# Kernel optimization log

Measured on AMD Instinct MI355X. Metric: run time of the kernel, lower is better.

Reference implementation:

```python
import jax, jax.numpy as jnp
import numpy as np

STRIDES = (8, 16, 32, 64)
NUM_HEADS = 8
G = 4
P = 32
TAU_Z = 2.0
LVL_BASE = 3.0  # stride 8 == 2**3 maps to level 0


def decode_box(xyzr):
    scale = jnp.exp2(xyzr[..., 2:3])
    ratio = jnp.exp2(jnp.concatenate([-0.5 * xyzr[..., 3:4], 0.5 * xyzr[..., 3:4]], axis=-1))
    wh = scale * ratio
    xy = xyzr[..., 0:2]
    return jnp.concatenate([xy - 0.5 * wh, xy + 0.5 * wh], axis=-1)


def position_embedding(box, num_feats, temperature=10000.0):
    term = jnp.array([1000.0, 1000.0, 1.0, 1.0], dtype=box.dtype)
    token = box / term
    dim_t = jnp.arange(num_feats, dtype=jnp.float32)
    dim_t = temperature ** (2.0 * (dim_t // 2) / num_feats)
    pos = token[..., None] / dim_t  # B,N,4,F
    pos = jnp.stack([jnp.sin(pos[..., 0::2]), jnp.cos(pos[..., 1::2])], axis=4)
    B, N = box.shape[:2]
    return pos.reshape(B, N, -1)  # B,N,4*F


def bbox_iof(boxes):
    # boxes: B,N,4 x1y1x2y2; iof[b,i,j] = inter(i,j) / area(i)
    area = jnp.clip(boxes[..., 2] - boxes[..., 0], 0.0) * jnp.clip(boxes[..., 3] - boxes[..., 1], 0.0)
    lt = jnp.maximum(boxes[:, :, None, :2], boxes[:, None, :, :2])
    rb = jnp.minimum(boxes[:, :, None, 2:], boxes[:, None, :, 2:])
    wh = jnp.clip(rb - lt, 0.0)
    inter = wh[..., 0] * wh[..., 1]
    return inter / jnp.clip(area[:, :, None], 1e-7, None)


def bilinear_group_sample(feat, xy, stride):
    # feat: [B,C,H,W]; xy: [B,N,P,G,2] image coords -> [B,N,G,P,C//G]
    B, C, H, W = feat.shape
    _, N, Pn, Gn, _ = xy.shape
    Cg = C // Gn
    featg = feat.reshape(B, Gn, Cg, H * W).transpose(0, 1, 3, 2)  # B,G,HW,Cg
    px = xy[..., 0] / stride - 0.5  # grid_sample align_corners=False convention
    py = xy[..., 1] / stride - 0.5
    x0 = jnp.floor(px)
    y0 = jnp.floor(py)
    bi = jnp.arange(B)[:, None, None]
    gi = jnp.arange(Gn)[None, :, None]
    out = jnp.zeros((B, Gn, N * Pn, Cg), dtype=feat.dtype)
    for dx in (0.0, 1.0):
        for dy in (0.0, 1.0):
            xi = x0 + dx
            yi = y0 + dy
            wgt = (1.0 - jnp.abs(px - xi)) * (1.0 - jnp.abs(py - yi))
            valid = (xi >= 0) & (xi <= W - 1) & (yi >= 0) & (yi <= H - 1)
            wgt = wgt * valid  # zero padding outside
            xi_c = jnp.clip(xi, 0, W - 1).astype(jnp.int32)
            yi_c = jnp.clip(yi, 0, H - 1).astype(jnp.int32)
            idx = (yi_c * W + xi_c).transpose(0, 3, 1, 2).reshape(B, Gn, N * Pn)
            vals = featg[bi, gi, idx]  # B,G,N*P,Cg
            w = wgt.transpose(0, 3, 1, 2).reshape(B, Gn, N * Pn, 1)
            out = out + vals * w
    return out.reshape(B, Gn, N, Pn, Cg).transpose(0, 2, 1, 3, 4)


def layer_norm(x, g, b, eps=1e-5):
    mu = jnp.mean(x, axis=-1, keepdims=True)
    var = jnp.mean((x - mu) ** 2, axis=-1, keepdims=True)
    return (x - mu) * jax.lax.rsqrt(var + eps) * g + b


def _forward(feats, query_content, query_box, Wq, bq, Wk, bk, Wv, bv, Wo, bo,
             ln_g, ln_b, off_W, off_b, sc_W, sc_b, iof_tau):
    B, N, C = query_content.shape
    H = NUM_HEADS
    dh = C // H
    box_cxcy = query_box[..., :2]
    zc = query_box[..., 2:3]
    rc = query_box[..., 3:4]
    box_wh = jnp.exp2(zc) * jnp.exp2(jnp.concatenate([-0.5 * rc, 0.5 * rc], axis=-1))
    logscale = zc.reshape(B, N, 1, 1)

    # torch.no_grad() block -> stop_gradient
    rois = decode_box(query_box)
    iof = jnp.log(bbox_iof(jax.lax.stop_gradient(rois)) + 1e-7)  # B,N,N
    pe = jax.lax.stop_gradient(position_embedding(query_box, C // 4))  # B,N,C
    attn_bias = iof[:, None, :, :] * iof_tau.reshape(1, -1, 1, 1)  # B,H,N,N

    x = query_content + pe
    q = (x @ Wq.T + bq).reshape(B, N, H, dh)
    k = (x @ Wk.T + bk).reshape(B, N, H, dh)
    v = (x @ Wv.T + bv).reshape(B, N, H, dh)
    scores = jnp.einsum('bnhd,bmhd->bhnm', q, k) * (dh ** -0.5) + attn_bias
    attn = jax.nn.softmax(scores, axis=-1)
    ctx = jnp.einsum('bhnm,bmhd->bnhd', attn, v).reshape(B, N, C)
    qc = x + ctx @ Wo.T + bo  # mmcv MultiheadAttention adds identity (= query+pe)
    qc = layer_norm(qc, ln_g, ln_b)

    offset = (qc @ off_W.T + off_b).reshape(B, N, P, G, 2)
    scale_logit = (qc @ sc_W.T + sc_b).reshape(B, N, P, G)
    sample_xy = box_cxcy.reshape(B, N, 1, 1, 2) + offset * box_wh.reshape(B, N, 1, 1, 2)
    sample_z = scale_logit + logscale  # B,N,P,G
    lvl = sample_z - LVL_BASE
    levels = jnp.arange(len(STRIDES), dtype=jnp.float32)
    zw = jax.nn.softmax(-((lvl[..., None] - levels) ** 2) / TAU_Z, axis=-1)  # B,N,P,G,L
    zw_t = zw.transpose(0, 1, 3, 2, 4)  # B,N,G,P,L
    sample_feats = jnp.zeros(())
    for l, (fm, s) in enumerate(zip(feats, STRIDES)):
        sample_feats = sample_feats + bilinear_group_sample(fm, sample_xy, s) * zw_t[..., l:l + 1]
    return sample_feats, sample_xy, offset, sample_z, scale_logit, qc


def setup_inputs():
    key = jax.random.key(0)
    ks = jax.random.split(key, 20)
    B, N, C = 4, 500, 256
    feat0 = jax.random.normal(ks[0], (B, C, 128, 128), dtype=jnp.float32)
    feat1 = jax.random.normal(ks[1], (B, C, 64, 64), dtype=jnp.float32)
    feat2 = jax.random.normal(ks[2], (B, C, 32, 32), dtype=jnp.float32)
    feat3 = jax.random.normal(ks[3], (B, C, 16, 16), dtype=jnp.float32)
    query_content = jax.random.normal(ks[4], (B, N, C), dtype=jnp.float32)
    xy = jax.random.uniform(ks[5], (B, N, 2), minval=64.0, maxval=960.0)
    zz = jax.random.uniform(ks[6], (B, N, 1), minval=3.0, maxval=6.0)
    rr = jax.random.uniform(ks[7], (B, N, 1), minval=-1.0, maxval=1.0)
    query_box = jnp.concatenate([xy, zz, rr], axis=-1)
    sub_query_xy = jax.random.normal(ks[8], (B, N, P, G, 2), dtype=jnp.float32) * 0.1
    sub_query_z = jax.random.normal(ks[9], (B, N, P, G, 4), dtype=jnp.float32) * 0.1
    sub_query_vec = jax.random.normal(ks[10], (B, N, P, G, 64), dtype=jnp.float32) * 0.1
    imgs_whwh = jnp.full((B, N, 4), 1024.0, dtype=jnp.float32)
    w = lambda i, sh: jax.random.normal(ks[i], sh, dtype=jnp.float32) * 0.02
    return {
        'feat0': feat0, 'feat1': feat1, 'feat2': feat2, 'feat3': feat3,
        'query_content': query_content, 'query_box': query_box,
        'sub_query_xy': sub_query_xy, 'sub_query_z': sub_query_z,
        'sub_query_vec': sub_query_vec, 'imgs_whwh': imgs_whwh,
        'Wq': w(11, (C, C)), 'bq': jnp.zeros((C,), jnp.float32),
        'Wk': w(12, (C, C)), 'bk': jnp.zeros((C,), jnp.float32),
        'Wv': w(13, (C, C)), 'bv': jnp.zeros((C,), jnp.float32),
        'Wo': w(14, (C, C)), 'bo': jnp.zeros((C,), jnp.float32),
        'ln_g': jnp.ones((C,), jnp.float32), 'ln_b': jnp.zeros((C,), jnp.float32),
        'off_W': w(15, (2 * G * P, C)),
        'off_b': jax.random.uniform(ks[16], (2 * G * P,), minval=-0.5, maxval=0.5),
        'sc_W': w(17, (G * P, C)),
        'sc_b': jax.random.normal(ks[18], (G * P,), dtype=jnp.float32) * 0.1,
        'iof_tau': jax.random.uniform(ks[19], (NUM_HEADS,), minval=0.0, maxval=4.0),
    }


def reference(feat0, feat1, feat2, feat3, query_content, query_box, sub_query_xy,
              sub_query_z, sub_query_vec, imgs_whwh, Wq, bq, Wk, bk, Wv, bv, Wo, bo,
              ln_g, ln_b, off_W, off_b, sc_W, sc_b, iof_tau):
    sample_feats, sample_xy, offset, sample_z, scale_logit, qc = _forward(
        [feat0, feat1, feat2, feat3], query_content, query_box,
        Wq, bq, Wk, bk, Wv, bv, Wo, bo, ln_g, ln_b, off_W, off_b, sc_W, sc_b, iof_tau)
    return (sample_feats, sub_query_xy, sub_query_z, sub_query_vec, qc,
            sample_xy, offset, sample_z, scale_logit)
```

## Files before the change

kernel.cpp:

```cpp
#include <hip/hip_runtime.h>
#include <cstdint>
#include <cstddef>

#define B_ 4
#define N_ 500
#define C_ 256
#define NH_ 8
#define DH_ 32
#define P_ 32
#define G_ 4
#define CG_ 64
#define BN_ (B_*N_)
#define QKV_QI 8

__constant__ const int LVL_W[4] = {128, 64, 32, 16};

static __device__ __forceinline__ unsigned short f2bf(float f) {
  union { float f; unsigned u; } v; v.f = f;
  unsigned r = v.u + 0x7FFF + ((v.u >> 16) & 1);
  return (unsigned short)(r >> 16);
}
static __device__ __forceinline__ float bf2f(unsigned u16shifted) {
  union { unsigned u; float f; } v; v.u = u16shifted;
  return v.f;
}

__global__ __launch_bounds__(256) void mega_kernel(
    const float* __restrict__ f0, const float* __restrict__ f1,
    const float* __restrict__ f2, const float* __restrict__ f3,
    unsigned short* __restrict__ t0, unsigned short* __restrict__ t1,
    unsigned short* __restrict__ t2, unsigned short* __restrict__ t3) {
  __shared__ unsigned short tile[64][260];
  int blk = blockIdx.x;
  int t = threadIdx.x;
  const float* src; unsigned short* dst; int npix, i;
  if (blk < 1024)      { src = f0; dst = t0; npix = 16384; i = blk; }
  else if (blk < 1280) { src = f1; dst = t1; npix = 4096;  i = blk - 1024; }
  else if (blk < 1344) { src = f2; dst = t2; npix = 1024;  i = blk - 1280; }
  else                 { src = f3; dst = t3; npix = 256;   i = blk - 1344; }
  int pb = npix >> 8;
  int px0 = (i % pb) * 256;
  int c0 = ((i / pb) & 3) * 64;
  int b  = i / (pb * 4);
  int lane = t & 63;
  int wv = t >> 6;
#pragma unroll
  for (int k = 0; k < 16; k++) {
    int r = k * 4 + wv;
    float4 v = *(const float4*)&src[((size_t)b * C_ + c0 + r) * npix + px0 + lane * 4];
    ushort4 u;
    u.x = f2bf(v.x); u.y = f2bf(v.y); u.z = f2bf(v.z); u.w = f2bf(v.w);
    int col = (lane * 4) ^ (((r >> 4) & 3) << 2);
    *(ushort4*)&tile[r][col] = u;
  }
  __syncthreads();
  int cq = t & 15;
  int pr = t >> 4;
#pragma unroll
  for (int k = 0; k < 16; k++) {
    int p = k * 16 + pr;
    ushort4 r4;
    {
      int ch = cq * 4;
      r4.x = tile[ch + 0][p ^ ((((ch + 0) >> 4) & 3) << 2)];
      r4.y = tile[ch + 1][p ^ ((((ch + 1) >> 4) & 3) << 2)];
      r4.z = tile[ch + 2][p ^ ((((ch + 2) >> 4) & 3) << 2)];
      r4.w = tile[ch + 3][p ^ ((((ch + 3) >> 4) & 3) << 2)];
    }
    *(ushort4*)&dst[((size_t)b * npix + px0 + p) * C_ + c0 + cq * 4] = r4;
  }
}

__global__ __launch_bounds__(256) void qkv_prep_kernel(
    const float* __restrict__ qcontent, const float* __restrict__ qbox,
    const float* __restrict__ Wq, const float* __restrict__ bq,
    const float* __restrict__ Wk, const float* __restrict__ bk,
    const float* __restrict__ Wv, const float* __restrict__ bv,
    float* __restrict__ x, float* __restrict__ boxd,
    float* __restrict__ q, float* __restrict__ kT, float* __restrict__ vT) {
  __shared__ float xs[QKV_QI][C_];
  int blk = blockIdx.x;
  int t = threadIdx.x;
  int bn0 = blk * QKV_QI;
  int d = t >> 6;
  float tj = exp2f((float)((t >> 1) & 31) * 0.4152410f);
  float tmul = (d < 2) ? 0.001f : 1.0f;
  for (int i = 0; i < QKV_QI; i++) {
    float qv = qbox[(size_t)(bn0 + i) * 4 + d];
    float val = qv * tmul / tj;
    float pe = (t & 1) ? cosf(val) : sinf(val);
    float xv = qcontent[(size_t)(bn0 + i) * C_ + t] + pe;
    xs[i][t] = xv;
    x[(size_t)(bn0 + i) * C_ + t] = xv;
  }
  if (t < QKV_QI) {
    int bn = bn0 + t;
    const float* qb = qbox + (size_t)bn * 4;
    float cx = qb[0], cy = qb[1], z = qb[2], r = qb[3];
    float scale = exp2f(z);
    float w = scale * exp2f(-0.5f * r);
    float h = scale * exp2f(0.5f * r);
    float* bd = boxd + (size_t)bn * 12;
    float x1 = cx - 0.5f * w, y1 = cy - 0.5f * h, x2 = cx + 0.5f * w, y2 = cy + 0.5f * h;
    bd[0] = x1; bd[1] = y1; bd[2] = x2; bd[3] = y2;
    bd[4] = cx; bd[5] = cy; bd[6] = w; bd[7] = h; bd[8] = z;
    float area = fmaxf(x2 - x1, 0.f) * fmaxf(y2 - y1, 0.f);
    bd[9] = fmaxf(area, 1e-7f);
  }
  __syncthreads();
  float accq[QKV_QI], acck[QKV_QI], accv[QKV_QI];
  for (int i = 0; i < QKV_QI; i++) { accq[i] = 0.f; acck[i] = 0.f; accv[i] = 0.f; }
  const float4* wq4 = (const float4*)(Wq + (size_t)t * C_);
  const float4* wk4 = (const float4*)(Wk + (size_t)t * C_);
  const float4* wv4 = (const float4*)(Wv + (size_t)t * C_);
  for (int k4 = 0; k4 < C_ / 4; k4++) {
    float4 wq = wq4[k4], wk = wk4[k4], wv = wv4[k4];
    for (int i = 0; i < QKV_QI; i++) {
      float4 xv = *(const float4*)&xs[i][k4 * 4];
      accq[i] += xv.x * wq.x + xv.y * wq.y + xv.z * wq.z + xv.w * wq.w;
      acck[i] += xv.x * wk.x + xv.y * wk.y + xv.z * wk.z + xv.w * wk.w;
      accv[i] += xv.x * wv.x + xv.y * wv.y + xv.z * wv.z + xv.w * wv.w;
    }
  }
  for (int i = 0; i < QKV_QI; i++) {
    int bn = bn0 + i;
    int b = bn / N_;
    int n = bn % N_;
    q[(size_t)bn * C_ + t] = accq[i] + bq[t];
    kT[((size_t)b * C_ + t) * N_ + n] = acck[i] + bk[t];
    vT[((size_t)b * C_ + t) * N_ + n] = accv[i] + bv[t];
  }
}

__global__ __launch_bounds__(256) void score_copy_kernel(
    const float* __restrict__ q, const float* __restrict__ kT,
    const float* __restrict__ boxd, const float* __restrict__ tau_p,
    float* __restrict__ S, float* __restrict__ Mpart,
    const float* __restrict__ subxy, const float* __restrict__ subz,
    const float* __restrict__ subv,
    float* __restrict__ o_subxy, float* __restrict__ o_subz,
    float* __restrict__ o_subv) {
  int blk = blockIdx.x;
  int t = threadIdx.x;
  if (blk >= 512) {
    int cb = blk - 512;
    const float4* s4; float4* d4;
    if (cb < 125)      { s4 = (const float4*)subxy + (size_t)cb * 1024;
                         d4 = (float4*)o_subxy + (size_t)cb * 1024; }
    else if (cb < 375) { s4 = (const float4*)subz + (size_t)(cb - 125) * 1024;
                         d4 = (float4*)o_subz + (size_t)(cb - 125) * 1024; }
    else               { s4 = (const float4*)subv + (size_t)(cb - 375) * 1024;
                         d4 = (float4*)o_subv + (size_t)(cb - 375) * 1024; }
    d4[t] = s4[t];
    d4[t + 256] = s4[t + 256];
    d4[t + 512] = s4[t + 512];
    d4[t + 768] = s4[t + 768];
    return;
  }
  int mp = (blk >> 1) & 7;
  int npar = blk & 1;
  int h = (blk >> 4) & 7;
  int b = blk >> 7;
  int w = t >> 6;
  int lane = t & 63;
  int m = mp * 64 + lane;
  int mc = min(m, N_ - 1);
  bool mok = m < N_;
  float tau = tau_p[h];
  const float scl = 0.17677669529663687f;

  float kreg[DH_];
  const float* kbase = kT + ((size_t)b * C_ + h * DH_) * N_ + mc;
#pragma unroll
  for (int d = 0; d < DH_; d++) kreg[d] = kbase[(size_t)d * N_];

  const float* bm = boxd + ((size_t)b * N_ + mc) * 12;
  float kx1 = bm[0], ky1 = bm[1], kx2 = bm[2], ky2 = bm[3];

  size_t srow_base = ((size_t)(b * NH_ + h)) * N_;
  for (int n = npar * 4 + w; n < N_; n += 8) {
    const float* qn = q + ((size_t)b * N_ + n) * C_ + h * DH_;
    float4 q0 = *(const float4*)&qn[0];
    float4 q1 = *(const float4*)&qn[4];
    float4 q2 = *(const float4*)&qn[8];
    float4 q3 = *(const float4*)&qn[12];
    float4 q4 = *(const float4*)&qn[16];
    float4 q5 = *(const float4*)&qn[20];
    float4 q6 = *(const float4*)&qn[24];
    float4 q7 = *(const float4*)&qn[28];
    float s0 = q0.x*kreg[0] + q0.y*kreg[1] + q0.z*kreg[2] + q0.w*kreg[3];
    float s1 = q1.x*kreg[4] + q1.y*kreg[5] + q1.z*kreg[6] + q1.w*kreg[7];
    float s2 = q2.x*kreg[8] + q2.y*kreg[9] + q2.z*kreg[10] + q2.w*kreg[11];
    float s3 = q3.x*kreg[12] + q3.y*kreg[13] + q3.z*kreg[14] + q3.w*kreg[15];
    s0 += q4.x*kreg[16] + q4.y*kreg[17] + q4.z*kreg[18] + q4.w*kreg[19];
    s1 += q5.x*kreg[20] + q5.y*kreg[21] + q5.z*kreg[22] + q5.w*kreg[23];
    s2 += q6.x*kreg[24] + q6.y*kreg[25] + q6.z*kreg[26] + q6.w*kreg[27];
    s3 += q7.x*kreg[28] + q7.y*kreg[29] + q7.z*kreg[30] + q7.w*kreg[31];
    float s = (s0 + s1) + (s2 + s3);

    const float* bn = boxd + ((size_t)b * N_ + n) * 12;
    float4 nb = *(const float4*)&bn[0];
    float inv_area = 1.0f / bn[9];
    float iw = fmaxf(fminf(nb.z, kx2) - fmaxf(nb.x, kx1), 0.f);
    float ih = fmaxf(fminf(nb.w, ky2) - fmaxf(nb.y, ky1), 0.f);
    float bias = logf(iw * ih * inv_area + 1e-7f);
    float sc = s * scl + bias * tau;

    if (mok) S[(srow_base + n) * 512 + m] = sc;
    float wm = mok ? sc : -1e30f;
#pragma unroll
    for (int off = 32; off >= 1; off >>= 1) wm = fmaxf(wm, __shfl_xor(wm, off, 64));
    if (lane == 0) Mpart[(srow_base + n) * 8 + mp] = wm;
  }
}

__global__ __launch_bounds__(256) void pv_kernel(
    const float* __restrict__ S, const float* __restrict__ Mpart,
    const float* __restrict__ vT, float* __restrict__ ctx) {
  int w = threadIdx.x >> 6;
  int lane = threadIdx.x & 63;
  int n0 = blockIdx.x * 4;
  int h = blockIdx.y * 4 + w;
  int b = blockIdx.z;
  size_t rb = ((size_t)(b * NH_ + h)) * N_;

  float mval = -1e30f;
  if (lane < 32) mval = Mpart[(rb + n0 + (lane >> 3)) * 8 + (lane & 7)];
  mval = fmaxf(mval, __shfl_xor(mval, 1, 64));
  mval = fmaxf(mval, __shfl_xor(mval, 2, 64));
  mval = fmaxf(mval, __shfl_xor(mval, 4, 64));
  float mx[4];
#pragma unroll
  for (int n = 0; n < 4; n++) mx[n] = __shfl(mval, n * 8, 64);

  float p[4][8];
  float inv[4];
#pragma unroll
  for (int n = 0; n < 4; n++) {
    const float* Srow = S + (rb + n0 + n) * 512;
    float sum = 0.f;
#pragma unroll
    for (int i = 0; i < 8; i++) {
      int m = lane + 64 * i;
      float sv = Srow[min(m, N_ - 1)];
      float e = (m < N_) ? __expf(sv - mx[n]) : 0.f;
      p[n][i] = e;
      sum += e;
    }
#pragma unroll
    for (int off = 32; off >= 1; off >>= 1) sum += __shfl_xor(sum, off, 64);
    inv[n] = 1.0f / sum;
  }

  const float* vbase = vT + ((size_t)b * C_ + h * DH_) * N_;
  float keep0 = 0.f, keep1 = 0.f, keep2 = 0.f, keep3 = 0.f;
  for (int cc = 0; cc < DH_; cc++) {
    const float* vrow = vbase + (size_t)cc * N_;
    float a0 = 0.f, a1 = 0.f, a2 = 0.f, a3 = 0.f;
#pragma unroll
    for (int i = 0; i < 8; i++) {
      int m = lane + 64 * i;
      float vv = vrow[min(m, N_ - 1)];
      a0 += p[0][i] * vv;
      a1 += p[1][i] * vv;
      a2 += p[2][i] * vv;
      a3 += p[3][i] * vv;
    }
#pragma unroll
    for (int off = 32; off >= 1; off >>= 1) {
      a0 += __shfl_xor(a0, off, 64);
      a1 += __shfl_xor(a1, off, 64);
      a2 += __shfl_xor(a2, off, 64);
      a3 += __shfl_xor(a3, off, 64);
    }
    bool sel = (lane & 31) == cc;
    keep0 = sel ? a0 : keep0;
    keep1 = sel ? a1 : keep1;
    keep2 = sel ? a2 : keep2;
    keep3 = sel ? a3 : keep3;
  }
  int c = lane & 31;
  size_t obase = ((size_t)b * N_ + n0) * C_ + h * DH_ + c;
  if (lane < 32) {
    ctx[obase + 0 * C_] = keep0 * inv[0];
    ctx[obase + 2 * C_] = keep2 * inv[2];
  } else {
    ctx[obase + 1 * C_] = keep1 * inv[1];
    ctx[obase + 3 * C_] = keep3 * inv[3];
  }
}

#define PQI 4
__global__ __launch_bounds__(256) void projln_head_kernel(
    const float* __restrict__ ctx, const float* __restrict__ x,
    const float* __restrict__ Wo, const float* __restrict__ bo,
    const float* __restrict__ ln_g, const float* __restrict__ ln_b,
    const float* __restrict__ boxd,
    const float* __restrict__ offW, const float* __restrict__ offb,
    const float* __restrict__ scW, const float* __restrict__ scb,
    float* __restrict__ qc_out,
    float* __restrict__ out_offset, float* __restrict__ out_sxy,
    float* __restrict__ out_sz, float* __restrict__ out_sl,
    float* __restrict__ zw_ws) {
  __shared__ float cs[PQI][C_];
  __shared__ float qs[PQI][C_];
  __shared__ float redbuf[PQI][8];
  int blk = blockIdx.x;
  int t = threadIdx.x;
  int bn0 = blk * PQI;
  for (int i = 0; i < PQI; i++) cs[i][t] = ctx[(size_t)(bn0 + i) * C_ + t];
  __syncthreads();
  float acc[PQI] = {0.f, 0.f, 0.f, 0.f};
  {
    const float4* w4 = (const float4*)(Wo + (size_t)t * C_);
    for (int k4 = 0; k4 < C_ / 4; k4++) {
      float4 w = w4[k4];
      for (int i = 0; i < PQI; i++) {
        float4 cv = *(const float4*)&cs[i][k4 * 4];
        acc[i] += cv.x * w.x + cv.y * w.y + cv.z * w.z + cv.w * w.w;
      }
    }
  }
  float y[PQI];
  int wave = t >> 6, lane = t & 63;
  for (int i = 0; i < PQI; i++) {
    y[i] = x[(size_t)(bn0 + i) * C_ + t] + acc[i] + bo[t];
    float s1 = y[i], s2 = y[i] * y[i];
#pragma unroll
    for (int off = 32; off >= 1; off >>= 1) {
      s1 += __shfl_xor(s1, off, 64);
      s2 += __shfl_xor(s2, off, 64);
    }
    if (lane == 0) { redbuf[i][wave] = s1; redbuf[i][wave + 4] = s2; }
  }
  __syncthreads();
  for (int i = 0; i < PQI; i++) {
    float s1 = redbuf[i][0] + redbuf[i][1] + redbuf[i][2] + redbuf[i][3];
    float s2 = redbuf[i][4] + redbuf[i][5] + redbuf[i][6] + redbuf[i][7];
    float mu = s1 * (1.0f / C_);
    float var = s2 * (1.0f / C_) - mu * mu;
    float inv = rsqrtf(var + 1e-5f);
    float o = (y[i] - mu) * inv * ln_g[t] + ln_b[t];
    qs[i][t] = o;
    qc_out[(size_t)(bn0 + i) * C_ + t] = o;
  }
  __syncthreads();
  float ao[PQI] = {0.f, 0.f, 0.f, 0.f};
  {
    const float4* w4 = (const float4*)(offW + (size_t)t * C_);
    for (int k4 = 0; k4 < C_ / 4; k4++) {
      float4 w = w4[k4];
      for (int i = 0; i < PQI; i++) {
        float4 cv = *(const float4*)&qs[i][k4 * 4];
        ao[i] += cv.x * w.x + cv.y * w.y + cv.z * w.z + cv.w * w.w;
      }
    }
  }
  int xy = t & 1;
  for (int i = 0; i < PQI; i++) {
    int bn = bn0 + i;
    const float* bd = boxd + (size_t)bn * 12;
    float off = ao[i] + offb[t];
    float ctr = xy ? bd[5] : bd[4];
    float wh = xy ? bd[7] : bd[6];
    float sxy = ctr + off * wh;
    out_offset[(size_t)bn * 256 + t] = off;
    out_sxy[(size_t)bn * 256 + t] = sxy;
  }
  if (t < 128) {
    float as[PQI] = {0.f, 0.f, 0.f, 0.f};
    const float4* sw4 = (const float4*)(scW + (size_t)t * C_);
    for (int k4 = 0; k4 < C_ / 4; k4++) {
      float4 w = sw4[k4];
      for (int i = 0; i < PQI; i++) {
        float4 cv = *(const float4*)&qs[i][k4 * 4];
        as[i] += cv.x * w.x + cv.y * w.y + cv.z * w.z + cv.w * w.w;
      }
    }
    for (int i = 0; i < PQI; i++) {
      int bn = bn0 + i;
      const float* bd = boxd + (size_t)bn * 12;
      float sl = as[i] + scb[t];
      float sz = sl + bd[8];
      out_sl[(size_t)bn * 128 + t] = sl;
      out_sz[(size_t)bn * 128 + t] = sz;
      float lvl = sz - 3.0f;
      float d1 = lvl - 1.f, d2 = lvl - 2.f, d3 = lvl - 3.f;
      float e0 = __expf(-0.5f * lvl * lvl);
      float e1 = __expf(-0.5f * d1 * d1);
      float e2 = __expf(-0.5f * d2 * d2);
      float e3 = __expf(-0.5f * d3 * d3);
      float inv = 1.0f / (e0 + e1 + e2 + e3);
      float* zw = zw_ws + ((size_t)bn * 128 + t) * 4;
      zw[0] = e0 * inv; zw[1] = e1 * inv; zw[2] = e2 * inv; zw[3] = e3 * inv;
    }
  }
}

__global__ __launch_bounds__(256) void sample_kernel_v3(
    const unsigned short* __restrict__ f0, const unsigned short* __restrict__ f1,
    const unsigned short* __restrict__ f2, const unsigned short* __restrict__ f3,
    const float* __restrict__ sxy, const float* __restrict__ zw_ws,
    float* __restrict__ out) {
  int t = threadIdx.x;
  int wv = t >> 6;
  int lane = t & 63;
  int sub = lane >> 4;
  int c4 = lane & 15;
  int pt = blockIdx.x * 16 + wv * 4 + sub;
  int g = pt & 3;
  int p = (pt >> 2) & 31;
  int bn = pt >> 7;
  int b = bn / N_;

  float sx = sxy[(size_t)pt * 2];
  float sy = sxy[(size_t)pt * 2 + 1];
  const float* zw = zw_ws + (size_t)pt * 4;
  const unsigned short* feats[4] = {f0, f1, f2, f3};
  const float inv_stride[4] = {0.125f, 0.0625f, 0.03125f, 0.015625f};
  float4 acc = {0.f, 0.f, 0.f, 0.f};
#pragma unroll
  for (int l = 0; l < 4; l++) {
    float wl = zw[l];
    int W = LVL_W[l];
    float px = sx * inv_stride[l] - 0.5f;
    float py = sy * inv_stride[l] - 0.5f;
    float x0f = floorf(px), y0f = floorf(py);
    float fx = px - x0f, fy = py - y0f;
    int x0 = (int)x0f, y0 = (int)y0f;
    const unsigned short* fb = feats[l] + (size_t)b * W * W * C_ + g * CG_ + c4 * 4;
#pragma unroll
    for (int dy = 0; dy < 2; dy++) {
#pragma unroll
      for (int dx = 0; dx < 2; dx++) {
        int xi = x0 + dx, yi = y0 + dy;
        float valid = (xi >= 0 && xi < W && yi >= 0 && yi < W) ? 1.f : 0.f;
        int xc = min(max(xi, 0), W - 1);
        int yc = min(max(yi, 0), W - 1);
        float wgt = (dx ? fx : 1.f - fx) * (dy ? fy : 1.f - fy) * valid * wl;
        uint2 u = *(const uint2*)&fb[((size_t)yc * W + xc) * C_];
        acc.x += wgt * bf2f(u.x << 16);
        acc.y += wgt * bf2f(u.x & 0xFFFF0000u);
        acc.z += wgt * bf2f(u.y << 16);
        acc.w += wgt * bf2f(u.y & 0xFFFF0000u);
      }
    }
  }
  *(float4*)&out[(size_t)bn * 8192 + g * 2048 + p * 64 + c4 * 4] = acc;
}

__global__ __launch_bounds__(256) void sample_kernel_native(
    const float* __restrict__ f0, const float* __restrict__ f1,
    const float* __restrict__ f2, const float* __restrict__ f3,
    const float* __restrict__ sxy, const float* __restrict__ zw_ws,
    float* __restrict__ out) {
  int t = threadIdx.x;
  int wv = t >> 6;
  int lane = t & 63;
  int pt = blockIdx.x * 4 + wv;
  int g = pt & 3;
  int p = (pt >> 2) & 31;
  int bn = pt >> 7;
  int b = bn / N_;
  float sx = sxy[(size_t)pt * 2];
  float sy = sxy[(size_t)pt * 2 + 1];
  const float* zw = zw_ws + (size_t)pt * 4;
  const float* feats[4] = {f0, f1, f2, f3};
  const float inv_stride[4] = {0.125f, 0.0625f, 0.03125f, 0.015625f};
  float acc = 0.f;
#pragma unroll
  for (int l = 0; l < 4; l++) {
    float wl = zw[l];
    int W = LVL_W[l];
    float px = sx * inv_stride[l] - 0.5f;
    float py = sy * inv_stride[l] - 0.5f;
    float x0f = floorf(px), y0f = floorf(py);
    float fx = px - x0f, fy = py - y0f;
    int x0 = (int)x0f, y0 = (int)y0f;
#pragma unroll
    for (int dy = 0; dy < 2; dy++) {
#pragma unroll
      for (int dx = 0; dx < 2; dx++) {
        int xi = x0 + dx, yi = y0 + dy;
        if (xi >= 0 && xi < W && yi >= 0 && yi < W) {
          float wgt = (dx ? fx : 1.f - fx) * (dy ? fy : 1.f - fy);
          float v = feats[l][(((size_t)b * C_ + g * CG_ + lane) * W + yi) * W + xi];
          acc += wgt * wl * v;
        }
      }
    }
  }
  out[(size_t)bn * 8192 + g * 2048 + p * 64 + lane] = acc;
}

extern "C" void kernel_launch(void* const* d_in, const int* in_sizes, int n_in,
                              void* d_out, int out_size, void* d_ws, size_t ws_size,
                              hipStream_t stream) {
  (void)in_sizes; (void)n_in; (void)out_size;
  const float* feat[4] = {(const float*)d_in[0], (const float*)d_in[1],
                          (const float*)d_in[2], (const float*)d_in[3]};
  const float* query_content = (const float*)d_in[4];
  const float* query_box = (const float*)d_in[5];
  const float* Wq = (const float*)d_in[10]; const float* bq = (const float*)d_in[11];
  const float* Wk = (const float*)d_in[12]; const float* bk = (const float*)d_in[13];
  const float* Wv = (const float*)d_in[14]; const float* bv = (const float*)d_in[15];
  const float* Wo = (const float*)d_in[16]; const float* bo = (const float*)d_in[17];
  const float* ln_g = (const float*)d_in[18]; const float* ln_b = (const float*)d_in[19];
  const float* offW = (const float*)d_in[20]; const float* offb = (const float*)d_in[21];
  const float* scW = (const float*)d_in[22]; const float* scb = (const float*)d_in[23];
  const float* iof_tau = (const float*)d_in[24];

  float* out = (float*)d_out;
  float* ws = (float*)d_ws;

  const size_t O_FEATS = 0;
  const size_t O_SUBXY = 16384000;
  const size_t O_SUBZ = 16896000;
  const size_t O_SUBV = 17920000;
  const size_t O_QC = 34304000;
  const size_t O_SXY = 34816000;
  const size_t O_OFF = 35328000;
  const size_t O_SZ = 35840000;
  const size_t O_SL = 36096000;

  float* S = out + O_FEATS;
  float* Mpart = out + O_FEATS + 8192000;

  const size_t o_x = 0;
  const size_t o_boxd = o_x + 512000;
  const size_t o_q = o_boxd + 24000;
  const size_t o_kT = o_q + 512000;
  const size_t o_vT = o_kT + 512000;
  const size_t o_ctx = o_vT + 512000;
  const size_t o_zw = o_ctx + 512000;
  const size_t o_ft = o_zw + 1024000;
  const size_t ft_sz[4] = {16777216, 4194304, 1048576, 262144};
  const size_t ft_total = ft_sz[0] + ft_sz[1] + ft_sz[2] + ft_sz[3];
  const size_t need_T = o_ft * sizeof(float) + ft_total * sizeof(unsigned short);
  const bool useT = ws_size >= need_T;

  unsigned short* ftu = (unsigned short*)(ws + o_ft);
  unsigned short* ftb[4] = {ftu,
                            ftu + ft_sz[0],
                            ftu + ft_sz[0] + ft_sz[1],
                            ftu + ft_sz[0] + ft_sz[1] + ft_sz[2]};

  if (useT) {
    mega_kernel<<<1360, 256, 0, stream>>>(
        feat[0], feat[1], feat[2], feat[3],
        ftb[0], ftb[1], ftb[2], ftb[3]);
  }

  qkv_prep_kernel<<<BN_ / QKV_QI, 256, 0, stream>>>(
      query_content, query_box, Wq, bq, Wk, bk, Wv, bv,
      ws + o_x, ws + o_boxd, ws + o_q, ws + o_kT, ws + o_vT);

  score_copy_kernel<<<512 + 4375, 256, 0, stream>>>(
      ws + o_q, ws + o_kT, ws + o_boxd, iof_tau, S, Mpart,
      (const float*)d_in[6], (const float*)d_in[7], (const float*)d_in[8],
      out + O_SUBXY, out + O_SUBZ, out + O_SUBV);

  {
    dim3 gb(N_ / 4, 2, B_);
    pv_kernel<<<gb, 256, 0, stream>>>(S, Mpart, ws + o_vT, ws + o_ctx);
  }

  projln_head_kernel<<<BN_ / PQI, 256, 0, stream>>>(
      ws + o_ctx, ws + o_x, Wo, bo, ln_g, ln_b, ws + o_boxd,
      offW, offb, scW, scb,
      out + O_QC, out + O_OFF, out + O_SXY, out + O_SZ, out + O_SL,
      ws + o_zw);

  const int npoints = BN_ * P_ * G_;
  if (useT) {
    sample_kernel_v3<<<npoints / 16, 256, 0, stream>>>(
        ftb[0], ftb[1], ftb[2], ftb[3],
        out + O_SXY, ws + o_zw, out + O_FEATS);
  } else {
    sample_kernel_native<<<npoints / 4, 256, 0, stream>>>(
        feat[0], feat[1], feat[2], feat[3],
        out + O_SXY, ws + o_zw, out + O_FEATS);
  }
}
```

Before: 294.9 us.

## Fuse attention PV into projection/LayerNorm head and widen sample loads to 8 channels

Merges the softmax-PV kernel into the output projection, LayerNorm and head kernel. Each block now computes the context for 4 queries across all 8 heads (2 heads per wave) straight into shared memory, so the ctx workspace round trip and one launch go away. The bilinear sampling kernel also has each lane gather 8 bf16 channels with a 16-byte load instead of 4, halving the grid. The fused kernel has fewer blocks (500 vs 1000+500), each doing more serial work, which may reduce parallelism.

```diff
diff --git a/kernel.cpp b/kernel.cpp
--- a/kernel.cpp
+++ b/kernel.cpp
@@ -214,85 +214,10 @@
   }
 }
 
-__global__ __launch_bounds__(256) void pv_kernel(
+#define PQI 4
+__global__ __launch_bounds__(256) void pv_projln_kernel(
     const float* __restrict__ S, const float* __restrict__ Mpart,
-    const float* __restrict__ vT, float* __restrict__ ctx) {
-  int w = threadIdx.x >> 6;
-  int lane = threadIdx.x & 63;
-  int n0 = blockIdx.x * 4;
-  int h = blockIdx.y * 4 + w;
-  int b = blockIdx.z;
-  size_t rb = ((size_t)(b * NH_ + h)) * N_;
-
-  float mval = -1e30f;
-  if (lane < 32) mval = Mpart[(rb + n0 + (lane >> 3)) * 8 + (lane & 7)];
-  mval = fmaxf(mval, __shfl_xor(mval, 1, 64));
-  mval = fmaxf(mval, __shfl_xor(mval, 2, 64));
-  mval = fmaxf(mval, __shfl_xor(mval, 4, 64));
-  float mx[4];
-#pragma unroll
-  for (int n = 0; n < 4; n++) mx[n] = __shfl(mval, n * 8, 64);
-
-  float p[4][8];
-  float inv[4];
-#pragma unroll
-  for (int n = 0; n < 4; n++) {
-    const float* Srow = S + (rb + n0 + n) * 512;
-    float sum = 0.f;
-#pragma unroll
-    for (int i = 0; i < 8; i++) {
-      int m = lane + 64 * i;
-      float sv = Srow[min(m, N_ - 1)];
-      float e = (m < N_) ? __expf(sv - mx[n]) : 0.f;
-      p[n][i] = e;
-      sum += e;
-    }
-#pragma unroll
-    for (int off = 32; off >= 1; off >>= 1) sum += __shfl_xor(sum, off, 64);
-    inv[n] = 1.0f / sum;
-  }
-
-  const float* vbase = vT + ((size_t)b * C_ + h * DH_) * N_;
-  float keep0 = 0.f, keep1 = 0.f, keep2 = 0.f, keep3 = 0.f;
-  for (int cc = 0; cc < DH_; cc++) {
-    const float* vrow = vbase + (size_t)cc * N_;
-    float a0 = 0.f, a1 = 0.f, a2 = 0.f, a3 = 0.f;
-#pragma unroll
-    for (int i = 0; i < 8; i++) {
-      int m = lane + 64 * i;
-      float vv = vrow[min(m, N_ - 1)];
-      a0 += p[0][i] * vv;
-      a1 += p[1][i] * vv;
-      a2 += p[2][i] * vv;
-      a3 += p[3][i] * vv;
-    }
-#pragma unroll
-    for (int off = 32; off >= 1; off >>= 1) {
-      a0 += __shfl_xor(a0, off, 64);
-      a1 += __shfl_xor(a1, off, 64);
-      a2 += __shfl_xor(a2, off, 64);
-      a3 += __shfl_xor(a3, off, 64);
-    }
-    bool sel = (lane & 31) == cc;
-    keep0 = sel ? a0 : keep0;
-    keep1 = sel ? a1 : keep1;
-    keep2 = sel ? a2 : keep2;
-    keep3 = sel ? a3 : keep3;
-  }
-  int c = lane & 31;
-  size_t obase = ((size_t)b * N_ + n0) * C_ + h * DH_ + c;
-  if (lane < 32) {
-    ctx[obase + 0 * C_] = keep0 * inv[0];
-    ctx[obase + 2 * C_] = keep2 * inv[2];
-  } else {
-    ctx[obase + 1 * C_] = keep1 * inv[1];
-    ctx[obase + 3 * C_] = keep3 * inv[3];
-  }
-}
-
-#define PQI 4
-__global__ __launch_bounds__(256) void projln_head_kernel(
-    const float* __restrict__ ctx, const float* __restrict__ x,
+    const float* __restrict__ vT, const float* __restrict__ x,
     const float* __restrict__ Wo, const float* __restrict__ bo,
     const float* __restrict__ ln_g, const float* __restrict__ ln_b,
     const float* __restrict__ boxd,
@@ -305,24 +230,102 @@
   __shared__ float cs[PQI][C_];
   __shared__ float qs[PQI][C_];
   __shared__ float redbuf[PQI][8];
-  int blk = blockIdx.x;
   int t = threadIdx.x;
-  int bn0 = blk * PQI;
-  for (int i = 0; i < PQI; i++) cs[i][t] = ctx[(size_t)(bn0 + i) * C_ + t];
+  int w = t >> 6;
+  int lane = t & 63;
+  int n0 = blockIdx.x * PQI;
+  int b = blockIdx.y;
+  int h0 = w * 2;
+
+  float mval;
+  {
+    int pair = lane >> 3;
+    int q_ = pair >> 1, hh_ = pair & 1;
+    size_t rbp = ((size_t)(b * NH_ + h0 + hh_)) * N_;
+    mval = Mpart[(rbp + n0 + q_) * 8 + (lane & 7)];
+  }
+  mval = fmaxf(mval, __shfl_xor(mval, 1, 64));
+  mval = fmaxf(mval, __shfl_xor(mval, 2, 64));
+  mval = fmaxf(mval, __shfl_xor(mval, 4, 64));
+  float mx[PQI][2];
+#pragma unroll
+  for (int q_ = 0; q_ < PQI; q_++)
+#pragma unroll
+    for (int hh = 0; hh < 2; hh++)
+      mx[q_][hh] = __shfl(mval, (q_ * 2 + hh) * 8, 64);
+
+#pragma unroll
+  for (int hh = 0; hh < 2; hh++) {
+    size_t rb = ((size_t)(b * NH_ + h0 + hh)) * N_;
+    float p[PQI][8];
+    float inv[PQI];
+#pragma unroll
+    for (int n = 0; n < PQI; n++) {
+      const float* Srow = S + (rb + n0 + n) * 512;
+      float sum = 0.f;
+#pragma unroll
+      for (int i = 0; i < 8; i++) {
+        int m = lane + 64 * i;
+        float sv = Srow[min(m, N_ - 1)];
+        float e = (m < N_) ? __expf(sv - mx[n][hh]) : 0.f;
+        p[n][i] = e;
+        sum += e;
+      }
+#pragma unroll
+      for (int off = 32; off >= 1; off >>= 1) sum += __shfl_xor(sum, off, 64);
+      inv[n] = 1.0f / sum;
+    }
+    const float* vbase = vT + ((size_t)b * C_ + (h0 + hh) * DH_) * N_;
+    float keep0 = 0.f, keep1 = 0.f, keep2 = 0.f, keep3 = 0.f;
+    for (int cc = 0; cc < DH_; cc++) {
+      const float* vrow = vbase + (size_t)cc * N_;
+      float a0 = 0.f, a1 = 0.f, a2 = 0.f, a3 = 0.f;
+#pragma unroll
+      for (int i = 0; i < 8; i++) {
+        int m = lane + 64 * i;
+        float vv = vrow[min(m, N_ - 1)];
+        a0 += p[0][i] * vv;
+        a1 += p[1][i] * vv;
+        a2 += p[2][i] * vv;
+        a3 += p[3][i] * vv;
+      }
+#pragma unroll
+      for (int off = 32; off >= 1; off >>= 1) {
+        a0 += __shfl_xor(a0, off, 64);
+        a1 += __shfl_xor(a1, off, 64);
+        a2 += __shfl_xor(a2, off, 64);
+        a3 += __shfl_xor(a3, off, 64);
+      }
+      bool sel = (lane & 31) == cc;
+      keep0 = sel ? a0 : keep0;
+      keep1 = sel ? a1 : keep1;
+      keep2 = sel ? a2 : keep2;
+      keep3 = sel ? a3 : keep3;
+    }
+    int c = (h0 + hh) * DH_ + (lane & 31);
+    if (lane < 32) {
+      cs[0][c] = keep0 * inv[0];
+      cs[2][c] = keep2 * inv[2];
+    } else {
+      cs[1][c] = keep1 * inv[1];
+      cs[3][c] = keep3 * inv[3];
+    }
+  }
   __syncthreads();
+
+  int bn0 = b * N_ + n0;
   float acc[PQI] = {0.f, 0.f, 0.f, 0.f};
   {
     const float4* w4 = (const float4*)(Wo + (size_t)t * C_);
     for (int k4 = 0; k4 < C_ / 4; k4++) {
-      float4 w = w4[k4];
+      float4 wv = w4[k4];
       for (int i = 0; i < PQI; i++) {
         float4 cv = *(const float4*)&cs[i][k4 * 4];
-        acc[i] += cv.x * w.x + cv.y * w.y + cv.z * w.z + cv.w * w.w;
+        acc[i] += cv.x * wv.x + cv.y * wv.y + cv.z * wv.z + cv.w * wv.w;
       }
     }
   }
   float y[PQI];
-  int wave = t >> 6, lane = t & 63;
   for (int i = 0; i < PQI; i++) {
     y[i] = x[(size_t)(bn0 + i) * C_ + t] + acc[i] + bo[t];
     float s1 = y[i], s2 = y[i] * y[i];
@@ -331,7 +334,7 @@
       s1 += __shfl_xor(s1, off, 64);
       s2 += __shfl_xor(s2, off, 64);
     }
-    if (lane == 0) { redbuf[i][wave] = s1; redbuf[i][wave + 4] = s2; }
+    if (lane == 0) { redbuf[i][w] = s1; redbuf[i][w + 4] = s2; }
   }
   __syncthreads();
   for (int i = 0; i < PQI; i++) {
@@ -349,10 +352,10 @@
   {
     const float4* w4 = (const float4*)(offW + (size_t)t * C_);
     for (int k4 = 0; k4 < C_ / 4; k4++) {
-      float4 w = w4[k4];
+      float4 wv = w4[k4];
       for (int i = 0; i < PQI; i++) {
         float4 cv = *(const float4*)&qs[i][k4 * 4];
-        ao[i] += cv.x * w.x + cv.y * w.y + cv.z * w.z + cv.w * w.w;
+        ao[i] += cv.x * wv.x + cv.y * wv.y + cv.z * wv.z + cv.w * wv.w;
       }
     }
   }
@@ -371,10 +374,10 @@
     float as[PQI] = {0.f, 0.f, 0.f, 0.f};
     const float4* sw4 = (const float4*)(scW + (size_t)t * C_);
     for (int k4 = 0; k4 < C_ / 4; k4++) {
-      float4 w = sw4[k4];
+      float4 wv = sw4[k4];
       for (int i = 0; i < PQI; i++) {
         float4 cv = *(const float4*)&qs[i][k4 * 4];
-        as[i] += cv.x * w.x + cv.y * w.y + cv.z * w.z + cv.w * w.w;
+        as[i] += cv.x * wv.x + cv.y * wv.y + cv.z * wv.z + cv.w * wv.w;
       }
     }
     for (int i = 0; i < PQI; i++) {
@@ -397,7 +400,7 @@
   }
 }
 
-__global__ __launch_bounds__(256) void sample_kernel_v3(
+__global__ __launch_bounds__(256) void sample_kernel_v4(
     const unsigned short* __restrict__ f0, const unsigned short* __restrict__ f1,
     const unsigned short* __restrict__ f2, const unsigned short* __restrict__ f3,
     const float* __restrict__ sxy, const float* __restrict__ zw_ws,
@@ -405,9 +408,9 @@
   int t = threadIdx.x;
   int wv = t >> 6;
   int lane = t & 63;
-  int sub = lane >> 4;
-  int c4 = lane & 15;
-  int pt = blockIdx.x * 16 + wv * 4 + sub;
+  int sub = lane >> 3;
+  int c8 = lane & 7;
+  int pt = blockIdx.x * 32 + wv * 8 + sub;
   int g = pt & 3;
   int p = (pt >> 2) & 31;
   int bn = pt >> 7;
@@ -418,7 +421,8 @@
   const float* zw = zw_ws + (size_t)pt * 4;
   const unsigned short* feats[4] = {f0, f1, f2, f3};
   const float inv_stride[4] = {0.125f, 0.0625f, 0.03125f, 0.015625f};
-  float4 acc = {0.f, 0.f, 0.f, 0.f};
+  float acc0 = 0.f, acc1 = 0.f, acc2 = 0.f, acc3 = 0.f;
+  float acc4 = 0.f, acc5 = 0.f, acc6 = 0.f, acc7 = 0.f;
 #pragma unroll
   for (int l = 0; l < 4; l++) {
     float wl = zw[l];
@@ -428,7 +432,7 @@
     float x0f = floorf(px), y0f = floorf(py);
     float fx = px - x0f, fy = py - y0f;
     int x0 = (int)x0f, y0 = (int)y0f;
-    const unsigned short* fb = feats[l] + (size_t)b * W * W * C_ + g * CG_ + c4 * 4;
+    const unsigned short* fb = feats[l] + (size_t)b * W * W * C_ + g * CG_ + c8 * 8;
 #pragma unroll
     for (int dy = 0; dy < 2; dy++) {
 #pragma unroll
@@ -438,15 +442,23 @@
         int xc = min(max(xi, 0), W - 1);
         int yc = min(max(yi, 0), W - 1);
         float wgt = (dx ? fx : 1.f - fx) * (dy ? fy : 1.f - fy) * valid * wl;
-        uint2 u = *(const uint2*)&fb[((size_t)yc * W + xc) * C_];
-        acc.x += wgt * bf2f(u.x << 16);
-        acc.y += wgt * bf2f(u.x & 0xFFFF0000u);
-        acc.z += wgt * bf2f(u.y << 16);
-        acc.w += wgt * bf2f(u.y & 0xFFFF0000u);
-      }
-    }
-  }
-  *(float4*)&out[(size_t)bn * 8192 + g * 2048 + p * 64 + c4 * 4] = acc;
+        uint4 u = *(const uint4*)&fb[((size_t)yc * W + xc) * C_];
+        acc0 += wgt * bf2f(u.x << 16);
+        acc1 += wgt * bf2f(u.x & 0xFFFF0000u);
+        acc2 += wgt * bf2f(u.y << 16);
+        acc3 += wgt * bf2f(u.y & 0xFFFF0000u);
+        acc4 += wgt * bf2f(u.z << 16);
+        acc5 += wgt * bf2f(u.z & 0xFFFF0000u);
+        acc6 += wgt * bf2f(u.w << 16);
+        acc7 += wgt * bf2f(u.w & 0xFFFF0000u);
+      }
+    }
+  }
+  float* ob = &out[(size_t)bn * 8192 + g * 2048 + p * 64 + c8 * 8];
+  float4 o0 = {acc0, acc1, acc2, acc3};
+  float4 o1 = {acc4, acc5, acc6, acc7};
+  *(float4*)&ob[0] = o0;
+  *(float4*)&ob[4] = o1;
 }
 
 __global__ __launch_bounds__(256) void sample_kernel_native(
@@ -531,8 +543,7 @@
   const size_t o_q = o_boxd + 24000;
   const size_t o_kT = o_q + 512000;
   const size_t o_vT = o_kT + 512000;
-  const size_t o_ctx = o_vT + 512000;
-  const size_t o_zw = o_ctx + 512000;
+  const size_t o_zw = o_vT + 512000;
   const size_t o_ft = o_zw + 1024000;
   const size_t ft_sz[4] = {16777216, 4194304, 1048576, 262144};
   const size_t ft_total = ft_sz[0] + ft_sz[1] + ft_sz[2] + ft_sz[3];
@@ -561,19 +572,17 @@
       out + O_SUBXY, out + O_SUBZ, out + O_SUBV);
 
   {
-    dim3 gb(N_ / 4, 2, B_);
-    pv_kernel<<<gb, 256, 0, stream>>>(S, Mpart, ws + o_vT, ws + o_ctx);
-  }
-
-  projln_head_kernel<<<BN_ / PQI, 256, 0, stream>>>(
-      ws + o_ctx, ws + o_x, Wo, bo, ln_g, ln_b, ws + o_boxd,
-      offW, offb, scW, scb,
-      out + O_QC, out + O_OFF, out + O_SXY, out + O_SZ, out + O_SL,
-      ws + o_zw);
+    dim3 gb(N_ / PQI, B_);
+    pv_projln_kernel<<<gb, 256, 0, stream>>>(
+        S, Mpart, ws + o_vT, ws + o_x, Wo, bo, ln_g, ln_b, ws + o_boxd,
+        offW, offb, scW, scb,
+        out + O_QC, out + O_OFF, out + O_SXY, out + O_SZ, out + O_SL,
+        ws + o_zw);
+  }
 
   const int npoints = BN_ * P_ * G_;
   if (useT) {
-    sample_kernel_v3<<<npoints / 16, 256, 0, stream>>>(
+    sample_kernel_v4<<<npoints / 32, 256, 0, stream>>>(
         ftb[0], ftb[1], ftb[2], ftb[3],
         out + O_SXY, ws + o_zw, out + O_FEATS);
   } else {
```

Measured after the change: 284.3 us. 3.6% less time.
